# Performance work log

Measured on AMD Instinct MI355X. Metric: run time of the kernel, lower is better.

The kernel has to match this reference:

```python
import jax, jax.numpy as jnp
import numpy as np

CHUNK_SIZE = 2048
EPS = 1e-12  # torch F.normalize clamps the norm at 1e-12


def _l2_normalize(x, axis):
    n = jnp.sqrt(jnp.sum(x * x, axis=axis, keepdims=True))
    return x / jnp.maximum(n, EPS)


def _nnfm_loss(F_r, F_s, chunk_size=CHUNK_SIZE):
    B, C, H_r, W_r = F_r.shape
    _, _, H_s, W_s = F_s.shape
    N_r = H_r * W_r
    N_s = H_s * W_s
    assert N_r % chunk_size == 0, "N_r must be divisible by chunk_size for this reference"
    n_chunks = N_r // chunk_size

    F_s_norm = _l2_normalize(F_s.reshape(B, C, N_s), axis=1)  # (B, C, N_s)
    F_r_flat = F_r.reshape(B, C, N_r)
    # (n_chunks, B, C, chunk) -- contiguous chunks along N_r, matching the torch loop
    chunks = F_r_flat.reshape(B, C, n_chunks, chunk_size).transpose(2, 0, 1, 3)

    def body(chunk):  # chunk: (B, C, chunk_size)
        cn = _l2_normalize(chunk, axis=1)
        sim = jnp.einsum('bcn,bcm->bnm', cn, F_s_norm)  # (B, chunk, N_s)
        # min(1 - sim) over N_s == 1 - max(sim)
        return 1.0 - jnp.max(sim, axis=2)  # (B, chunk)

    min_dists = jax.lax.map(body, chunks)  # (n_chunks, B, chunk) -- bounded memory
    return jnp.mean(min_dists)


def setup_inputs() -> dict:
    key = jax.random.key(0)
    k1, k2 = jax.random.split(key)
    F_r = jax.random.normal(k1, (1, 768, 128, 128), dtype=jnp.float32)
    F_s = jax.random.normal(k2, (1, 768, 128, 128), dtype=jnp.float32)
    return {"F_r": F_r, "F_s": F_s}


def reference(F_r, F_s):
    return _nnfm_loss(F_r, F_s)
```

## Files before the change

kernel.cpp:

```cpp
#include <hip/hip_runtime.h>
#include <cstdint>
#include <cstddef>

#define C_DIM 768
#define N_DIM 16384

typedef __attribute__((ext_vector_type(4))) int i32x4;

__device__ __forceinline__ void async_ld16(const void* g, void* l) {
    __builtin_amdgcn_global_load_lds(
        (__attribute__((address_space(1))) void*)g,
        (__attribute__((address_space(3))) void*)l,
        16, 0, 0);
}

__global__ __launch_bounds__(256) void norm_q(const float* __restrict__ F0,
                                              signed char* __restrict__ Q0,
                                              float* __restrict__ S0,
                                              const float* __restrict__ F1,
                                              signed char* __restrict__ Q1,
                                              float* __restrict__ S1) {
    const float*  F = blockIdx.y ? F1 : F0;
    signed char*  Q = blockIdx.y ? Q1 : Q0;
    float*        S = blockIdx.y ? S1 : S0;
    const int i0 = blockIdx.x * 64;
    const int t  = threadIdx.x;
    const int tx = t & 63;
    const int ty = t >> 6;

    float ss = 0.f, mx = 0.f;
    for (int c = ty; c < C_DIM; c += 4) {
        float v = F[(size_t)c * N_DIM + i0 + tx];
        ss += v * v;
        mx = fmaxf(mx, fabsf(v));
    }
    __shared__ float red_s[4][64];
    __shared__ float red_m[4][64];
    __shared__ float qscale[64];
    red_s[ty][tx] = ss;
    red_m[ty][tx] = mx;
    __syncthreads();
    if (t < 64) {
        float s = red_s[0][t] + red_s[1][t] + red_s[2][t] + red_s[3][t];
        float m = fmaxf(fmaxf(red_m[0][t], red_m[1][t]),
                        fmaxf(red_m[2][t], red_m[3][t]));
        float n = fmaxf(sqrtf(s), 1e-12f);
        qscale[t] = 127.0f / m;
        S[i0 + t] = m / (127.0f * n);
    }
    __syncthreads();

    __shared__ float tile[64][65];
    const int i_l   = t >> 3;
    const int c_off = (t & 7) * 8;
    for (int c0 = 0; c0 < C_DIM; c0 += 64) {
        #pragma unroll
        for (int rr = 0; rr < 16; ++rr) {
            int c_l = rr * 4 + ty;
            tile[c_l][tx] = F[(size_t)(c0 + c_l) * N_DIM + i0 + tx] * qscale[tx];
        }
        __syncthreads();
        #pragma unroll
        for (int half = 0; half < 2; ++half) {
            int il = i_l + half * 32;
            unsigned lo = 0, hi = 0;
            #pragma unroll
            for (int j = 0; j < 4; ++j) {
                int q = __float2int_rn(tile[c_off + j][il]);
                lo |= (unsigned)(q & 0xff) << (8 * j);
            }
            #pragma unroll
            for (int j = 0; j < 4; ++j) {
                int q = __float2int_rn(tile[c_off + 4 + j][il]);
                hi |= (unsigned)(q & 0xff) << (8 * j);
            }
            uint2 u; u.x = lo; u.y = hi;
            *(uint2*)&Q[(size_t)(i0 + il) * C_DIM + c0 + c_off] = u;
        }
        __syncthreads();
    }
}

__global__ __launch_bounds__(512) void gemm_rowmax(const signed char* __restrict__ A,
                                                   const signed char* __restrict__ B,
                                                   const float* __restrict__ sA,
                                                   const float* __restrict__ sB,
                                                   unsigned* __restrict__ rowkey) {
    __shared__ __align__(16) signed char As[2][128 * 64];
    __shared__ __align__(16) signed char Bs[2][256 * 64];

    const int t    = threadIdx.x;
    const int lane = t & 63;
    const int w    = t >> 6;
    const int wm   = w >> 2;
    const int wn   = w & 3;

    const int bid   = blockIdx.x;
    const int xcd   = bid & 7;
    const int local = bid >> 3;
    const int m0    = (local >> 3) * 128;
    const int n0    = (xcd * 8 + (local & 7)) * 256;

    i32x4 acc[4][4];
    #pragma unroll
    for (int i = 0; i < 4; ++i)
        #pragma unroll
        for (int j = 0; j < 4; ++j)
            acc[i][j] = (i32x4){0, 0, 0, 0};

    const int kq = ((t & 3) ^ ((t >> 3) & 3)) * 16;
    const signed char* ag  = A + (size_t)(m0 + (t >> 2)) * C_DIM + kq;
    const signed char* bg0 = B + (size_t)(n0 + (t >> 2)) * C_DIM + kq;
    const signed char* bg1 = bg0 + (size_t)128 * C_DIM;
    const int lda  = t * 16;
    const int ldb0 = t * 16, ldb1 = 128 * 64 + t * 16;

    const int qp    = ((lane >> 4) ^ ((lane >> 1) & 3)) * 16;
    const int a_off = (wm * 64 + (lane & 15)) * 64 + qp;
    const int b_off = (wn * 64 + (lane & 15)) * 64 + qp;

    async_ld16(ag,  As[0] + lda);
    async_ld16(bg0, Bs[0] + ldb0);
    async_ld16(bg1, Bs[0] + ldb1);

    int buf = 0;
    for (int k0 = 0; k0 < C_DIM; k0 += 64) {
        __syncthreads();
        if (k0 + 64 < C_DIM) {
            const int kn = k0 + 64, nb = buf ^ 1;
            async_ld16(ag + kn,  As[nb] + lda);
            async_ld16(bg0 + kn, Bs[nb] + ldb0);
            async_ld16(bg1 + kn, Bs[nb] + ldb1);
        }

        const signed char* Ab = As[buf];
        const signed char* Bb = Bs[buf];
        i32x4 af[4], bfr[4];
        #pragma unroll
        for (int mt = 0; mt < 4; ++mt)
            af[mt] = *(const i32x4*)(Ab + a_off + mt * 16 * 64);
        #pragma unroll
        for (int nt = 0; nt < 4; ++nt)
            bfr[nt] = *(const i32x4*)(Bb + b_off + nt * 16 * 64);
        #pragma unroll
        for (int mt = 0; mt < 4; ++mt)
            #pragma unroll
            for (int nt = 0; nt < 4; ++nt)
                acc[mt][nt] = __builtin_amdgcn_mfma_i32_16x16x64_i8(
                    af[mt], bfr[nt], acc[mt][nt], 0, 0, 0);
        buf ^= 1;
    }

    float sb[4];
    #pragma unroll
    for (int nt = 0; nt < 4; ++nt)
        sb[nt] = sB[n0 + wn * 64 + nt * 16 + (lane & 15)];

    #pragma unroll
    for (int mt = 0; mt < 4; ++mt) {
        #pragma unroll
        for (int reg = 0; reg < 4; ++reg) {
            float v = fmaxf(fmaxf((float)acc[mt][0][reg] * sb[0],
                                  (float)acc[mt][1][reg] * sb[1]),
                            fmaxf((float)acc[mt][2][reg] * sb[2],
                                  (float)acc[mt][3][reg] * sb[3]));
            #pragma unroll
            for (int off = 1; off < 16; off <<= 1)
                v = fmaxf(v, __shfl_xor(v, off, 64));
            if ((lane & 15) == 0) {
                int m = m0 + wm * 64 + mt * 16 + (lane >> 4) * 4 + reg;
                v *= sA[m];
                unsigned u = __float_as_uint(v);
                u = (u & 0x80000000u) ? ~u : (u | 0x80000000u);
                atomicMax(&rowkey[m], u);
            }
        }
    }
}

__global__ __launch_bounds__(1024) void finalize(const unsigned* __restrict__ rowkey,
                                                 float* __restrict__ out) {
    const int t = threadIdx.x;
    float s = 0.f;
    for (int i = t; i < N_DIM; i += 1024) {
        unsigned u = rowkey[i];
        float f = (u & 0x80000000u) ? __uint_as_float(u ^ 0x80000000u)
                                    : __uint_as_float(~u);
        s += f;
    }
    #pragma unroll
    for (int off = 32; off >= 1; off >>= 1)
        s += __shfl_down(s, off, 64);
    __shared__ float part[16];
    if ((t & 63) == 0) part[t >> 6] = s;
    __syncthreads();
    if (t == 0) {
        float tot = 0.f;
        #pragma unroll
        for (int i = 0; i < 16; ++i) tot += part[i];
        out[0] = 1.0f - tot * (1.0f / (float)N_DIM);
    }
}

extern "C" void kernel_launch(void* const* d_in, const int* in_sizes, int n_in,
                              void* d_out, int out_size, void* d_ws, size_t ws_size,
                              hipStream_t stream) {
    const float* F_r = (const float*)d_in[0];
    const float* F_s = (const float*)d_in[1];

    signed char* Rq = (signed char*)d_ws;
    signed char* Sq = Rq + (size_t)N_DIM * C_DIM;
    float* sR       = (float*)(Sq + (size_t)N_DIM * C_DIM);
    float* sS       = sR + N_DIM;
    unsigned* rowkey= (unsigned*)(sS + N_DIM);
    float* out      = (float*)d_out;

    hipLaunchKernelGGL(norm_q, dim3(N_DIM / 64, 2), dim3(256), 0, stream,
                       F_r, Rq, sR, F_s, Sq, sS);
    hipMemsetAsync(rowkey, 0, N_DIM * sizeof(unsigned), stream);
    hipLaunchKernelGGL(gemm_rowmax, dim3((N_DIM / 128) * (N_DIM / 256)), dim3(512),
                       0, stream, Rq, Sq, sR, sS, rowkey);
    hipLaunchKernelGGL(finalize, dim3(1), dim3(1024), 0, stream, rowkey, out);
}
```

Measured before the change: 714.1 us.

## Keep full-K A panel resident in LDS and stream B with running row max

The GEMM now loads a 128-row, full-K int8 A panel into LDS once per block and loops over 32 N-tiles. B fragments are read directly from global memory into registers, and a running per-row max is kept across tiles. The grid shrinks to 256 persistent-style blocks, cutting LDS double-buffer traffic and reducing row-max atomics. The trade-off is exposed global-load latency for B with no LDS staging or prefetch, and large LDS use that limits occupancy to one block per CU.

```diff
diff --git a/kernel.cpp b/kernel.cpp
--- a/kernel.cpp
+++ b/kernel.cpp
@@ -81,101 +81,113 @@
     }
 }
 
-__global__ __launch_bounds__(512) void gemm_rowmax(const signed char* __restrict__ A,
-                                                   const signed char* __restrict__ B,
-                                                   const float* __restrict__ sA,
-                                                   const float* __restrict__ sB,
-                                                   unsigned* __restrict__ rowkey) {
-    __shared__ __align__(16) signed char As[2][128 * 64];
-    __shared__ __align__(16) signed char Bs[2][256 * 64];
-
-    const int t    = threadIdx.x;
-    const int lane = t & 63;
-    const int w    = t >> 6;
-    const int wm   = w >> 2;
-    const int wn   = w & 3;
-
-    const int bid   = blockIdx.x;
-    const int xcd   = bid & 7;
-    const int local = bid >> 3;
-    const int m0    = (local >> 3) * 128;
-    const int n0    = (xcd * 8 + (local & 7)) * 256;
-
-    i32x4 acc[4][4];
-    #pragma unroll
-    for (int i = 0; i < 4; ++i)
-        #pragma unroll
-        for (int j = 0; j < 4; ++j)
-            acc[i][j] = (i32x4){0, 0, 0, 0};
-
-    const int kq = ((t & 3) ^ ((t >> 3) & 3)) * 16;
-    const signed char* ag  = A + (size_t)(m0 + (t >> 2)) * C_DIM + kq;
-    const signed char* bg0 = B + (size_t)(n0 + (t >> 2)) * C_DIM + kq;
-    const signed char* bg1 = bg0 + (size_t)128 * C_DIM;
-    const int lda  = t * 16;
-    const int ldb0 = t * 16, ldb1 = 128 * 64 + t * 16;
-
-    const int qp    = ((lane >> 4) ^ ((lane >> 1) & 3)) * 16;
-    const int a_off = (wm * 64 + (lane & 15)) * 64 + qp;
-    const int b_off = (wn * 64 + (lane & 15)) * 64 + qp;
-
-    async_ld16(ag,  As[0] + lda);
-    async_ld16(bg0, Bs[0] + ldb0);
-    async_ld16(bg1, Bs[0] + ldb1);
-
-    int buf = 0;
-    for (int k0 = 0; k0 < C_DIM; k0 += 64) {
-        __syncthreads();
-        if (k0 + 64 < C_DIM) {
-            const int kn = k0 + 64, nb = buf ^ 1;
-            async_ld16(ag + kn,  As[nb] + lda);
-            async_ld16(bg0 + kn, Bs[nb] + ldb0);
-            async_ld16(bg1 + kn, Bs[nb] + ldb1);
-        }
-
-        const signed char* Ab = As[buf];
-        const signed char* Bb = Bs[buf];
-        i32x4 af[4], bfr[4];
+__global__ __launch_bounds__(512, 2) void gemm_rowmax(const signed char* __restrict__ A,
+                                                      const signed char* __restrict__ B,
+                                                      const float* __restrict__ sA,
+                                                      const float* __restrict__ sB,
+                                                      unsigned* __restrict__ rowkey) {
+    __shared__ __align__(16) signed char As[128 * C_DIM];
+
+    const int t     = threadIdx.x;
+    const int lane  = t & 63;
+    const int w     = t >> 6;
+    const int wm    = w >> 2;
+    const int wn    = w & 3;
+    const int row15 = lane & 15;
+    const int kc    = lane >> 4;
+    const int x7    = lane & 7;
+
+    const int bid = blockIdx.x;
+    const int h   = bid & 1;
+    const int m0  = (bid >> 1) * 128;
+
+    #pragma unroll
+    for (int i = 0; i < 12; ++i) {
+        int s   = i * 512 + t;
+        int row = s / 48;
+        int pc  = s - row * 48;
+        int lc  = (pc & ~7) | ((pc & 7) ^ (row & 7));
+        async_ld16(A + (size_t)(m0 + row) * C_DIM + lc * 16, As + s * 16);
+    }
+    __syncthreads();
+
+    const signed char* Bw = B + ((size_t)(h * 8192 + wn * 64 + row15)) * C_DIM
+                              + kc * 16;
+    const float* sBw = sB + h * 8192 + wn * 64 + row15;
+
+    float runmax[4][4];
+    #pragma unroll
+    for (int mt = 0; mt < 4; ++mt)
+        #pragma unroll
+        for (int reg = 0; reg < 4; ++reg)
+            runmax[mt][reg] = -1e30f;
+
+    for (int ntile = 0; ntile < 32; ++ntile) {
+        const signed char* Bt = Bw + (size_t)ntile * 256 * C_DIM;
+
+        i32x4 acc[4][4];
         #pragma unroll
         for (int mt = 0; mt < 4; ++mt)
-            af[mt] = *(const i32x4*)(Ab + a_off + mt * 16 * 64);
+            #pragma unroll
+            for (int nt = 0; nt < 4; ++nt)
+                acc[mt][nt] = (i32x4){0, 0, 0, 0};
+
+        #pragma unroll
+        for (int ks = 0; ks < 12; ++ks) {
+            i32x4 bfrag[4];
+            #pragma unroll
+            for (int nt = 0; nt < 4; ++nt)
+                bfrag[nt] = *(const i32x4*)(Bt + (size_t)nt * 16 * C_DIM + ks * 64);
+
+            const int c  = ks * 4 + kc;
+            const int pc = (c & ~7) | ((c & 7) ^ x7);
+            i32x4 afrag[4];
+            #pragma unroll
+            for (int mt = 0; mt < 4; ++mt)
+                afrag[mt] = *(const i32x4*)(As + (wm * 64 + mt * 16 + row15) * C_DIM
+                                               + pc * 16);
+
+            #pragma unroll
+            for (int mt = 0; mt < 4; ++mt)
+                #pragma unroll
+                for (int nt = 0; nt < 4; ++nt)
+                    acc[mt][nt] = __builtin_amdgcn_mfma_i32_16x16x64_i8(
+                        afrag[mt], bfrag[nt], acc[mt][nt], 0, 0, 0);
+        }
+
+        float sb[4];
         #pragma unroll
         for (int nt = 0; nt < 4; ++nt)
-            bfr[nt] = *(const i32x4*)(Bb + b_off + nt * 16 * 64);
+            sb[nt] = sBw[ntile * 256 + nt * 16];
+
         #pragma unroll
         for (int mt = 0; mt < 4; ++mt)
             #pragma unroll
-            for (int nt = 0; nt < 4; ++nt)
-                acc[mt][nt] = __builtin_amdgcn_mfma_i32_16x16x64_i8(
-                    af[mt], bfr[nt], acc[mt][nt], 0, 0, 0);
-        buf ^= 1;
-    }
-
-    float sb[4];
-    #pragma unroll
-    for (int nt = 0; nt < 4; ++nt)
-        sb[nt] = sB[n0 + wn * 64 + nt * 16 + (lane & 15)];
-
-    #pragma unroll
-    for (int mt = 0; mt < 4; ++mt) {
+            for (int reg = 0; reg < 4; ++reg) {
+                float v = fmaxf(fmaxf((float)acc[mt][0][reg] * sb[0],
+                                      (float)acc[mt][1][reg] * sb[1]),
+                                fmaxf((float)acc[mt][2][reg] * sb[2],
+                                      (float)acc[mt][3][reg] * sb[3]));
+                runmax[mt][reg] = fmaxf(runmax[mt][reg], v);
+            }
+    }
+
+    #pragma unroll
+    for (int mt = 0; mt < 4; ++mt)
         #pragma unroll
         for (int reg = 0; reg < 4; ++reg) {
-            float v = fmaxf(fmaxf((float)acc[mt][0][reg] * sb[0],
-                                  (float)acc[mt][1][reg] * sb[1]),
-                            fmaxf((float)acc[mt][2][reg] * sb[2],
-                                  (float)acc[mt][3][reg] * sb[3]));
+            float v = runmax[mt][reg];
             #pragma unroll
             for (int off = 1; off < 16; off <<= 1)
                 v = fmaxf(v, __shfl_xor(v, off, 64));
-            if ((lane & 15) == 0) {
-                int m = m0 + wm * 64 + mt * 16 + (lane >> 4) * 4 + reg;
+            if (row15 == 0) {
+                int m = m0 + wm * 64 + mt * 16 + kc * 4 + reg;
                 v *= sA[m];
                 unsigned u = __float_as_uint(v);
                 u = (u & 0x80000000u) ? ~u : (u | 0x80000000u);
                 atomicMax(&rowkey[m], u);
             }
         }
-    }
 }
 
 __global__ __launch_bounds__(1024) void finalize(const unsigned* __restrict__ rowkey,
@@ -218,7 +230,7 @@
     hipLaunchKernelGGL(norm_q, dim3(N_DIM / 64, 2), dim3(256), 0, stream,
                        F_r, Rq, sR, F_s, Sq, sS);
     hipMemsetAsync(rowkey, 0, N_DIM * sizeof(unsigned), stream);
-    hipLaunchKernelGGL(gemm_rowmax, dim3((N_DIM / 128) * (N_DIM / 256)), dim3(512),
-                       0, stream, Rq, Sq, sR, sS, rowkey);
+    hipLaunchKernelGGL(gemm_rowmax, dim3(256), dim3(512), 0, stream,
+                       Rq, Sq, sR, sS, rowkey);
     hipLaunchKernelGGL(finalize, dim3(1), dim3(1024), 0, stream, rowkey, out);
 }
```

Result: no change. 713.7 us (-0.1%).
